# Performance work log

Measured on AMD Instinct MI355X. Metric: run time of the kernel, lower is better.

The kernel has to match this reference:

```python
import jax, jax.numpy as jnp
import numpy as np

DIM = 128
N_HEADS = 4
HEAD_DIM = DIM // N_HEADS
K = 16
B, N = 2, 8192
BIAS_HID = 32


def knn_idx(xyz, k):
    # squared pairwise distances: [B,N,N] (same argsort order as cdist)
    sq = jnp.sum(xyz * xyz, axis=-1)  # [B,N]
    d2 = sq[:, :, None] + sq[:, None, :] - 2.0 * jnp.einsum('bnd,bmd->bnm', xyz, xyz)
    _, idx = jax.lax.top_k(-d2, k)  # smallest distances
    return idx  # [B,N,k]


def setup_inputs() -> dict:
    key = jax.random.key(0)
    ks = jax.random.split(key, 12)
    s = 1.0 / np.sqrt(DIM)
    inp = {
        'x':   jax.random.normal(ks[0], (B, N, DIM), jnp.float32),
        'xyz': jax.random.normal(ks[1], (B, N, 3), jnp.float32),
        'Wq': jax.random.uniform(ks[2], (DIM, DIM), jnp.float32, -s, s),
        'bq': jnp.zeros((DIM,), jnp.float32),
        'Wk': jax.random.uniform(ks[3], (DIM, DIM), jnp.float32, -s, s),
        'bk': jnp.zeros((DIM,), jnp.float32),
        'Wv': jax.random.uniform(ks[4], (DIM, DIM), jnp.float32, -s, s),
        'bv': jnp.zeros((DIM,), jnp.float32),
        'Wo': jax.random.uniform(ks[5], (DIM, DIM), jnp.float32, -s, s),
        'bo': jnp.zeros((DIM,), jnp.float32),
        'W1': jax.random.uniform(ks[6], (3, BIAS_HID), jnp.float32, -0.5, 0.5),
        'b1': jnp.zeros((BIAS_HID,), jnp.float32),
        'W2': jax.random.uniform(ks[7], (BIAS_HID, N_HEADS), jnp.float32, -1.0 / np.sqrt(BIAS_HID), 1.0 / np.sqrt(BIAS_HID)),
        'b2': jnp.zeros((N_HEADS,), jnp.float32),
    }
    return inp


def reference(x, xyz, Wq, bq, Wk, bk, Wv, bv, Wo, bo, W1, b1, W2, b2):
    Bb, Nn, C = x.shape
    idx = knn_idx(xyz, K)  # [B,N,k]

    q = (x @ Wq + bq).reshape(Bb, Nn, N_HEADS, HEAD_DIM)
    kf = (x @ Wk + bk).reshape(Bb, Nn, N_HEADS, HEAD_DIM)
    vf = (x @ Wv + bv).reshape(Bb, Nn, N_HEADS, HEAD_DIM)

    gather = jax.vmap(lambda f, i: f[i])  # per-batch fancy gather
    kn = gather(kf, idx)  # [B,N,k,H,D]
    vn = gather(vf, idx)  # [B,N,k,H,D]
    nxyz = gather(xyz, idx)  # [B,N,k,3]

    rel = xyz[:, :, None, :] - nxyz  # [B,N,k,3]
    bias = jax.nn.relu(rel @ W1 + b1) @ W2 + b2  # [B,N,k,H]

    scores = jnp.einsum('bnhd,bnkhd->bnhk', q, kn) / np.sqrt(HEAD_DIM)
    scores = scores + jnp.swapaxes(bias, 2, 3)  # [B,N,H,k]
    attn = jax.nn.softmax(scores, axis=-1)
    out = jnp.einsum('bnhk,bnkhd->bnhd', attn, vn).reshape(Bb, Nn, C)
    return out @ Wo + bo
```

## Files before the change

### kernel.cpp

```cpp
#include <hip/hip_runtime.h>
#include <hip/hip_bf16.h>
#include <math.h>

#define BATCH 2
#define NPT   8192
#define DIMC  128
#define NH    4
#define KNN_K 16
#define HID   32
#define BN    (BATCH*NPT)

#define TILE 1024
#define QPW  2
#define NWV  4

__device__ __forceinline__ float readlane_f(float v, int l) {
  return __int_as_float(__builtin_amdgcn_readlane(__float_as_int(v), l));
}

__global__ __launch_bounds__(256) void knn_kernel(const float* __restrict__ xyz,
                                                  int* __restrict__ knn_out) {
  __shared__ float4 spts[TILE];
  const int tid  = threadIdx.x;
  const int lane = tid & 63;
  const int wave = tid >> 6;
  const int qbase = blockIdx.x * (NWV*QPW) + wave * QPW;
  const int b = qbase / NPT;

  float qx[QPW], qy[QPW], qz[QPW], qsq[QPW];
  float topd[QPW]; int topi[QPW]; float tau[QPW];
#pragma unroll
  for (int qi = 0; qi < QPW; ++qi) {
    const int g = qbase + qi;
    qx[qi] = xyz[(size_t)g*3+0];
    qy[qi] = xyz[(size_t)g*3+1];
    qz[qi] = xyz[(size_t)g*3+2];
    qsq[qi] = __fadd_rn(__fadd_rn(__fmul_rn(qx[qi],qx[qi]),
                                  __fmul_rn(qy[qi],qy[qi])),
                        __fmul_rn(qz[qi],qz[qi]));
    topd[qi] = 3e38f; topi[qi] = 0; tau[qi] = 3e38f;
  }

  for (int t = 0; t < NPT/TILE; ++t) {
    __syncthreads();
    const float* src = xyz + (size_t)(b*NPT + t*TILE)*3;
    for (int i = tid; i < TILE; i += 256) {
      const float x = src[i*3+0], y = src[i*3+1], z = src[i*3+2];
      const float sq = __fadd_rn(__fadd_rn(__fmul_rn(x,x), __fmul_rn(y,y)),
                                 __fmul_rn(z,z));
      spts[i] = make_float4(x+x, y+y, z+z, sq);
    }
    __syncthreads();

    for (int c = 0; c < TILE/64; ++c) {
      const float4 cd = spts[c*64 + lane];
      const int cbase = t*TILE + c*64;
#pragma unroll
      for (int qi = 0; qi < QPW; ++qi) {
        float dot2 = __fadd_rn(__fadd_rn(__fmul_rn(qx[qi],cd.x),
                                         __fmul_rn(qy[qi],cd.y)),
                               __fmul_rn(qz[qi],cd.z));
        float d2 = __fsub_rn(__fadd_rn(qsq[qi], cd.w), dot2);
        unsigned long long m = __ballot(d2 < tau[qi]);
        while (m) {
          const int l = (int)__builtin_ctzll(m);
          const float dn = readlane_f(d2, l);
          const int   ni_ = cbase + l;
          const float my  = topd[qi];
          const int   myi = topi[qi];
          float ab  = __shfl_up(my, 1);
          int   abi = __shfl_up(myi, 1);
          if (lane == 0) ab = -3e38f;
          const bool ge = dn < my;
          const bool gt = dn < ab;
          topd[qi] = ge ? (gt ? ab  : dn ) : my;
          topi[qi] = ge ? (gt ? abi : ni_) : myi;
          tau[qi] = readlane_f(topd[qi], 15);
          m &= (m - 1);
          if (m) m &= __ballot(d2 < tau[qi]);
        }
      }
    }
  }

#pragma unroll
  for (int qi = 0; qi < QPW; ++qi) {
    if (lane < KNN_K) knn_out[(size_t)(qbase + qi)*KNN_K + lane] = topi[qi];
  }
}

__device__ __forceinline__ float f4c(const float4 v, int u) {
  return u == 0 ? v.x : u == 1 ? v.y : u == 2 ? v.z : v.w;
}

#define QKV_ROWS 32

__global__ __launch_bounds__(128) void qkv_kernel(const float* __restrict__ x,
    const float* __restrict__ Wq, const float* __restrict__ bq,
    const float* __restrict__ Wk, const float* __restrict__ bk,
    const float* __restrict__ Wv, const float* __restrict__ bv,
    float* __restrict__ q, float* __restrict__ k, float* __restrict__ v) {
  __shared__ float xs[QKV_ROWS*DIMC];
  const int tid = threadIdx.x;
  const int rowbase = blockIdx.x * QKV_ROWS;
  {
    float4* xs4 = (float4*)xs;
    const float4* src4 = (const float4*)(x + (size_t)rowbase*DIMC);
    for (int i = tid; i < QKV_ROWS*DIMC/4; i += 128) xs4[i] = src4[i];
  }
  __syncthreads();

  const int cg = tid & 31, rg = tid >> 5;
  const int c0 = cg * 4;
  float4 aq[8], ak[8], av[8];
  {
    const float4 bq4 = *(const float4*)&bq[c0];
    const float4 bk4 = *(const float4*)&bk[c0];
    const float4 bv4 = *(const float4*)&bv[c0];
#pragma unroll
    for (int i = 0; i < 8; ++i) { aq[i] = bq4; ak[i] = bk4; av[i] = bv4; }
  }

  for (int kk = 0; kk < DIMC; kk += 4) {
    float4 xr[8];
#pragma unroll
    for (int i = 0; i < 8; ++i)
      xr[i] = *(const float4*)&xs[(rg + 4*i)*DIMC + kk];
#pragma unroll
    for (int u = 0; u < 4; ++u) {
      const float4 wq = *(const float4*)&Wq[(size_t)(kk+u)*DIMC + c0];
      const float4 wk = *(const float4*)&Wk[(size_t)(kk+u)*DIMC + c0];
      const float4 wv = *(const float4*)&Wv[(size_t)(kk+u)*DIMC + c0];
#pragma unroll
      for (int i = 0; i < 8; ++i) {
        const float xv = f4c(xr[i], u);
        aq[i].x = fmaf(xv, wq.x, aq[i].x); aq[i].y = fmaf(xv, wq.y, aq[i].y);
        aq[i].z = fmaf(xv, wq.z, aq[i].z); aq[i].w = fmaf(xv, wq.w, aq[i].w);
        ak[i].x = fmaf(xv, wk.x, ak[i].x); ak[i].y = fmaf(xv, wk.y, ak[i].y);
        ak[i].z = fmaf(xv, wk.z, ak[i].z); ak[i].w = fmaf(xv, wk.w, ak[i].w);
        av[i].x = fmaf(xv, wv.x, av[i].x); av[i].y = fmaf(xv, wv.y, av[i].y);
        av[i].z = fmaf(xv, wv.z, av[i].z); av[i].w = fmaf(xv, wv.w, av[i].w);
      }
    }
  }

#pragma unroll
  for (int i = 0; i < 8; ++i) {
    const size_t rr = (size_t)(rowbase + rg + 4*i)*DIMC + c0;
    *(float4*)&q[rr] = aq[i];
    *(float4*)&k[rr] = ak[i];
    *(float4*)&v[rr] = av[i];
  }
}

template <int CTRL>
__device__ __forceinline__ float dppf(float x) {
  return __int_as_float(__builtin_amdgcn_update_dpp(
      __float_as_int(x), __float_as_int(x), CTRL, 0xF, 0xF, false));
}
#define ROR1 0x121
#define ROR2 0x122
#define ROR4 0x124
#define ROR8 0x128

__global__ __launch_bounds__(256) void attn_kernel(const float* __restrict__ xyz,
    const int* __restrict__ knn, const float* __restrict__ qb,
    const float* __restrict__ kb, const float* __restrict__ vb,
    const float* __restrict__ W1, const float* __restrict__ b1,
    const float* __restrict__ W2, const float* __restrict__ b2,
    float* __restrict__ ao) {
  __shared__ float sw[4][NH][KNN_K];
  __shared__ int   sn[4][KNN_K];
  const int tid  = threadIdx.x;
  const int wave = tid >> 6;
  const int lane = tid & 63;
  const int p = blockIdx.x * 4 + wave;
  const int b = p / NPT;
  const int h = lane >> 4;
  const int j = lane & 15;

  const int nj = knn[(size_t)p*KNN_K + j];
  if (h == 0) sn[wave][j] = nj;
  const size_t nn = (size_t)b*NPT + nj;

  const float qx0 = xyz[(size_t)p*3+0];
  const float qy0 = xyz[(size_t)p*3+1];
  const float qz0 = xyz[(size_t)p*3+2];
  const float rx = qx0 - xyz[nn*3+0];
  const float ry = qy0 - xyz[nn*3+1];
  const float rz = qz0 - xyz[nn*3+2];
  float bias = b2[h];
#pragma unroll 8
  for (int u = 0; u < HID; ++u) {
    float hv = rx*W1[0*HID+u] + ry*W1[1*HID+u] + rz*W1[2*HID+u] + b1[u];
    hv = hv > 0.f ? hv : 0.f;
    bias = fmaf(hv, W2[u*NH + h], bias);
  }

  const float* qrow = qb + (size_t)p*DIMC + h*32;
  const float* krow = kb + nn*DIMC + h*32;
  float s = 0.f;
#pragma unroll
  for (int u = 0; u < 32; u += 4) {
    const float4 qv = *(const float4*)(qrow + u);
    const float4 kv = *(const float4*)(krow + u);
    s = fmaf(qv.x, kv.x, s); s = fmaf(qv.y, kv.y, s);
    s = fmaf(qv.z, kv.z, s); s = fmaf(qv.w, kv.w, s);
  }
  s = s * 0.17677669529663689f + bias;

  float m = s;
  m = fmaxf(m, dppf<ROR1>(m));
  m = fmaxf(m, dppf<ROR2>(m));
  m = fmaxf(m, dppf<ROR4>(m));
  m = fmaxf(m, dppf<ROR8>(m));
  const float e = expf(s - m);
  float ssum = e;
  ssum += dppf<ROR1>(ssum);
  ssum += dppf<ROR2>(ssum);
  ssum += dppf<ROR4>(ssum);
  ssum += dppf<ROR8>(ssum);
  sw[wave][h][j] = e / ssum;

  __syncthreads();

  const int d0 = lane;
  const int hA = d0 >> 5;
  float out0 = 0.f, out1 = 0.f;
  const float* vbase = vb + (size_t)b*NPT*DIMC;
#pragma unroll 4
  for (int j2 = 0; j2 < KNN_K; ++j2) {
    const int n = sn[wave][j2];
    const float wA = sw[wave][hA][j2];
    const float wB = sw[wave][2+hA][j2];
    const float* vrow = vbase + (size_t)n*DIMC;
    out0 = fmaf(wA, vrow[d0],    out0);
    out1 = fmaf(wB, vrow[64+d0], out1);
  }
  ao[(size_t)p*DIMC + d0]      = out0;
  ao[(size_t)p*DIMC + 64 + d0] = out1;
}

__global__ __launch_bounds__(128) void proj_kernel(float* __restrict__ inout,
    const float* __restrict__ Wo, const float* __restrict__ bo) {
  __shared__ float xs[QKV_ROWS*DIMC];
  const int tid = threadIdx.x;
  const int rowbase = blockIdx.x * QKV_ROWS;
  {
    float4* xs4 = (float4*)xs;
    const float4* src4 = (const float4*)(inout + (size_t)rowbase*DIMC);
    for (int i = tid; i < QKV_ROWS*DIMC/4; i += 128) xs4[i] = src4[i];
  }
  __syncthreads();

  const int cg = tid & 31, rg = tid >> 5;
  const int c0 = cg * 4;
  float4 a[8];
  {
    const float4 bo4 = *(const float4*)&bo[c0];
#pragma unroll
    for (int i = 0; i < 8; ++i) a[i] = bo4;
  }

  for (int kk = 0; kk < DIMC; kk += 4) {
    float4 xr[8];
#pragma unroll
    for (int i = 0; i < 8; ++i)
      xr[i] = *(const float4*)&xs[(rg + 4*i)*DIMC + kk];
#pragma unroll
    for (int u = 0; u < 4; ++u) {
      const float4 w = *(const float4*)&Wo[(size_t)(kk+u)*DIMC + c0];
#pragma unroll
      for (int i = 0; i < 8; ++i) {
        const float xv = f4c(xr[i], u);
        a[i].x = fmaf(xv, w.x, a[i].x); a[i].y = fmaf(xv, w.y, a[i].y);
        a[i].z = fmaf(xv, w.z, a[i].z); a[i].w = fmaf(xv, w.w, a[i].w);
      }
    }
  }

#pragma unroll
  for (int i = 0; i < 8; ++i)
    *(float4*)&inout[(size_t)(rowbase + rg + 4*i)*DIMC + c0] = a[i];
}

extern "C" void kernel_launch(void* const* d_in, const int* in_sizes, int n_in,
                              void* d_out, int out_size, void* d_ws, size_t ws_size,
                              hipStream_t stream) {
  const float* x   = (const float*)d_in[0];
  const float* xyz = (const float*)d_in[1];
  const float* Wq  = (const float*)d_in[2];
  const float* bq  = (const float*)d_in[3];
  const float* Wk  = (const float*)d_in[4];
  const float* bk  = (const float*)d_in[5];
  const float* Wv  = (const float*)d_in[6];
  const float* bv  = (const float*)d_in[7];
  const float* Wo  = (const float*)d_in[8];
  const float* bo  = (const float*)d_in[9];
  const float* W1  = (const float*)d_in[10];
  const float* b1  = (const float*)d_in[11];
  const float* W2  = (const float*)d_in[12];
  const float* b2  = (const float*)d_in[13];
  float* out = (float*)d_out;

  char* ws = (char*)d_ws;
  int*   knn = (int*)ws;
  float* q   = (float*)(ws + (size_t)(1u<<20));
  float* k   = (float*)(ws + (size_t)9*(1u<<20));
  float* v   = (float*)(ws + (size_t)17*(1u<<20));

  hipLaunchKernelGGL(knn_kernel, dim3(BN/(NWV*QPW)), dim3(256), 0, stream, xyz, knn);
  hipLaunchKernelGGL(qkv_kernel, dim3(BN/QKV_ROWS), dim3(128), 0, stream,
                     x, Wq, bq, Wk, bk, Wv, bv, q, k, v);
  hipLaunchKernelGGL(attn_kernel, dim3(BN/4), dim3(256), 0, stream,
                     xyz, knn, q, k, v, W1, b1, W2, b2, out);
  hipLaunchKernelGGL(proj_kernel, dim3(BN/QKV_ROWS), dim3(128), 0, stream,
                     out, Wo, bo);
}
```

Before: 194.6 us.

## Replace brute-force KNN with uniform-grid spatial binning and ring search

Swaps the all-pairs KNN scan for a 32^3 uniform grid built per batch. Zero, count, scan and scatter kernels bin the points into cells, then a query kernel searches outward ring by ring around each query's cell and stops once the ring bound exceeds the current 16th-best distance. Distance ties are broken by index so the result stays deterministic. This removes the O(N^2) distance work in exchange for four extra small launches, a single-block scan and atomics, and the cell bounds assume coordinates mostly fall in [-4,4].

```diff
diff --git a/kernel.cpp b/kernel.cpp
--- a/kernel.cpp
+++ b/kernel.cpp
@@ -10,83 +10,152 @@
 #define HID   32
 #define BN    (BATCH*NPT)
 
-#define TILE 1024
-#define QPW  2
-#define NWV  4
+#define GRID_N 32
+#define NCELL  (GRID_N*GRID_N*GRID_N)
+#define GLO   -4.0f
+#define GCS    0.25f
+#define GINV   4.0f
 
 __device__ __forceinline__ float readlane_f(float v, int l) {
   return __int_as_float(__builtin_amdgcn_readlane(__float_as_int(v), l));
 }
-
-__global__ __launch_bounds__(256) void knn_kernel(const float* __restrict__ xyz,
-                                                  int* __restrict__ knn_out) {
-  __shared__ float4 spts[TILE];
-  const int tid  = threadIdx.x;
-  const int lane = tid & 63;
-  const int wave = tid >> 6;
-  const int qbase = blockIdx.x * (NWV*QPW) + wave * QPW;
-  const int b = qbase / NPT;
-
-  float qx[QPW], qy[QPW], qz[QPW], qsq[QPW];
-  float topd[QPW]; int topi[QPW]; float tau[QPW];
-#pragma unroll
-  for (int qi = 0; qi < QPW; ++qi) {
-    const int g = qbase + qi;
-    qx[qi] = xyz[(size_t)g*3+0];
-    qy[qi] = xyz[(size_t)g*3+1];
-    qz[qi] = xyz[(size_t)g*3+2];
-    qsq[qi] = __fadd_rn(__fadd_rn(__fmul_rn(qx[qi],qx[qi]),
-                                  __fmul_rn(qy[qi],qy[qi])),
-                        __fmul_rn(qz[qi],qz[qi]));
-    topd[qi] = 3e38f; topi[qi] = 0; tau[qi] = 3e38f;
-  }
-
-  for (int t = 0; t < NPT/TILE; ++t) {
+__device__ __forceinline__ int clampi(int v, int lo, int hi) {
+  return v < lo ? lo : (v > hi ? hi : v);
+}
+__device__ __forceinline__ int cell_of(float x, float y, float z) {
+  const int cx = clampi((int)floorf((x - GLO)*GINV), 0, GRID_N-1);
+  const int cy = clampi((int)floorf((y - GLO)*GINV), 0, GRID_N-1);
+  const int cz = clampi((int)floorf((z - GLO)*GINV), 0, GRID_N-1);
+  return (cz*GRID_N + cy)*GRID_N + cx;
+}
+
+__global__ __launch_bounds__(256) void zero_kernel(int* __restrict__ c) {
+  const int i = blockIdx.x*256 + threadIdx.x;
+  if (i < 2*NCELL) c[i] = 0;
+}
+
+__global__ __launch_bounds__(256) void count_kernel(const float* __restrict__ xyz,
+                                                    int* __restrict__ counts) {
+  const int i = blockIdx.x*256 + threadIdx.x;
+  const float x = xyz[(size_t)i*3+0], y = xyz[(size_t)i*3+1], z = xyz[(size_t)i*3+2];
+  const int b = i >> 13;
+  atomicAdd(&counts[b*NCELL + cell_of(x,y,z)], 1);
+}
+
+__global__ __launch_bounds__(1024) void scan_kernel(const int* __restrict__ counts,
+                                                    int* __restrict__ starts,
+                                                    int* __restrict__ cursor) {
+  __shared__ int sd[1024];
+  const int t = threadIdx.x;
+  for (int b = 0; b < 2; ++b) {
+    const int* c = counts + b*NCELL;
+    int* s  = starts + b*(NCELL+1);
+    int* cu = cursor + b*NCELL;
+    int loc[32]; int sum = 0;
+#pragma unroll
+    for (int j = 0; j < 32; ++j) { loc[j] = sum; sum += c[t*32 + j]; }
     __syncthreads();
-    const float* src = xyz + (size_t)(b*NPT + t*TILE)*3;
-    for (int i = tid; i < TILE; i += 256) {
-      const float x = src[i*3+0], y = src[i*3+1], z = src[i*3+2];
-      const float sq = __fadd_rn(__fadd_rn(__fmul_rn(x,x), __fmul_rn(y,y)),
-                                 __fmul_rn(z,z));
-      spts[i] = make_float4(x+x, y+y, z+z, sq);
-    }
+    sd[t] = sum;
     __syncthreads();
-
-    for (int c = 0; c < TILE/64; ++c) {
-      const float4 cd = spts[c*64 + lane];
-      const int cbase = t*TILE + c*64;
-#pragma unroll
-      for (int qi = 0; qi < QPW; ++qi) {
-        float dot2 = __fadd_rn(__fadd_rn(__fmul_rn(qx[qi],cd.x),
-                                         __fmul_rn(qy[qi],cd.y)),
-                               __fmul_rn(qz[qi],cd.z));
-        float d2 = __fsub_rn(__fadd_rn(qsq[qi], cd.w), dot2);
-        unsigned long long m = __ballot(d2 < tau[qi]);
-        while (m) {
-          const int l = (int)__builtin_ctzll(m);
-          const float dn = readlane_f(d2, l);
-          const int   ni_ = cbase + l;
-          const float my  = topd[qi];
-          const int   myi = topi[qi];
-          float ab  = __shfl_up(my, 1);
-          int   abi = __shfl_up(myi, 1);
-          if (lane == 0) ab = -3e38f;
-          const bool ge = dn < my;
-          const bool gt = dn < ab;
-          topd[qi] = ge ? (gt ? ab  : dn ) : my;
-          topi[qi] = ge ? (gt ? abi : ni_) : myi;
-          tau[qi] = readlane_f(topd[qi], 15);
-          m &= (m - 1);
-          if (m) m &= __ballot(d2 < tau[qi]);
+    for (int off = 1; off < 1024; off <<= 1) {
+      const int u = (t >= off) ? sd[t-off] : 0;
+      __syncthreads();
+      sd[t] += u;
+      __syncthreads();
+    }
+    const int excl = sd[t] - sum;
+#pragma unroll
+    for (int j = 0; j < 32; ++j) { s[t*32+j] = excl + loc[j]; cu[t*32+j] = excl + loc[j]; }
+    if (t == 1023) s[NCELL] = sd[1023];
+  }
+}
+
+__global__ __launch_bounds__(256) void scatter_kernel(const float* __restrict__ xyz,
+    int* __restrict__ cursor, float4* __restrict__ pts4, int* __restrict__ pidx) {
+  const int i = blockIdx.x*256 + threadIdx.x;
+  const float x = xyz[(size_t)i*3+0], y = xyz[(size_t)i*3+1], z = xyz[(size_t)i*3+2];
+  const int b = i >> 13;
+  const float sq = __fadd_rn(__fadd_rn(__fmul_rn(x,x), __fmul_rn(y,y)),
+                             __fmul_rn(z,z));
+  const int slot = atomicAdd(&cursor[b*NCELL + cell_of(x,y,z)], 1);
+  pts4[b*NPT + slot] = make_float4(x+x, y+y, z+z, sq);
+  pidx[b*NPT + slot] = i & (NPT-1);
+}
+
+__global__ __launch_bounds__(256) void knn_query_kernel(const float* __restrict__ xyz,
+    const int* __restrict__ starts, const float4* __restrict__ pts4,
+    const int* __restrict__ pidx, int* __restrict__ knn_out) {
+  const int tid = threadIdx.x, lane = tid & 63, wave = tid >> 6;
+  const int p = blockIdx.x*4 + wave;
+  const int b = p >> 13;
+  const float qx = xyz[(size_t)p*3+0], qy = xyz[(size_t)p*3+1], qz = xyz[(size_t)p*3+2];
+  const float qsq = __fadd_rn(__fadd_rn(__fmul_rn(qx,qx), __fmul_rn(qy,qy)),
+                              __fmul_rn(qz,qz));
+  const int cx = clampi((int)floorf((qx - GLO)*GINV), 0, GRID_N-1);
+  const int cy = clampi((int)floorf((qy - GLO)*GINV), 0, GRID_N-1);
+  const int cz = clampi((int)floorf((qz - GLO)*GINV), 0, GRID_N-1);
+  const int*    sb = starts + b*(NCELL+1);
+  const float4* pb = pts4 + (size_t)b*NPT;
+  const int*    ib = pidx + (size_t)b*NPT;
+
+  float topd = INFINITY; int topi = 0x7fffffff;
+  float tau  = INFINITY; int taui = 0x7fffffff;
+
+  auto process = [&](int beg, int end) {
+    for (int c0 = beg; c0 < end; c0 += 64) {
+      const int ci = c0 + lane;
+      float d2 = INFINITY; int di = 0x7fffffff;
+      if (ci < end) {
+        const float4 cd = pb[ci];
+        const float dot2 = __fadd_rn(__fadd_rn(__fmul_rn(qx,cd.x),
+                                               __fmul_rn(qy,cd.y)),
+                                     __fmul_rn(qz,cd.z));
+        d2 = __fsub_rn(__fadd_rn(qsq, cd.w), dot2);
+        di = ib[ci];
+      }
+      unsigned long long m = __ballot((d2 < tau) | (d2 == tau && di < taui));
+      while (m) {
+        const int l = (int)__builtin_ctzll(m);
+        const float dn  = readlane_f(d2, l);
+        const int   dni = __builtin_amdgcn_readlane(di, l);
+        const float my  = topd; const int myi = topi;
+        float ab  = __shfl_up(my, 1);
+        int   abi = __shfl_up(myi, 1);
+        if (lane == 0) { ab = -INFINITY; abi = -1; }
+        const bool ge = (dn < my) | (dn == my && dni < myi);
+        const bool gt = (dn < ab) | (dn == ab && dni < abi);
+        topd = ge ? (gt ? ab  : dn ) : my;
+        topi = ge ? (gt ? abi : dni) : myi;
+        tau  = readlane_f(topd, 15);
+        taui = __builtin_amdgcn_readlane(topi, 15);
+        m &= (m - 1);
+        if (m) m &= __ballot((d2 < tau) | (d2 == tau && di < taui));
+      }
+    }
+  };
+
+  for (int r = 0; r < GRID_N; ++r) {
+    const int zlo = clampi(cz-r, 0, GRID_N-1), zhi = clampi(cz+r, 0, GRID_N-1);
+    const int ylo = clampi(cy-r, 0, GRID_N-1), yhi = clampi(cy+r, 0, GRID_N-1);
+    const int xlo = clampi(cx-r, 0, GRID_N-1), xhi = clampi(cx+r, 0, GRID_N-1);
+    for (int z = zlo; z <= zhi; ++z) {
+      const bool ze = (z == cz-r) || (z == cz+r);
+      for (int y = ylo; y <= yhi; ++y) {
+        const bool ye = (y == cy-r) || (y == cy+r);
+        const int cb = (z*GRID_N + y)*GRID_N;
+        if (ze || ye) {
+          process(sb[cb+xlo], sb[cb+xhi+1]);
+        } else {
+          if (cx-r >= 0)       process(sb[cb+cx-r], sb[cb+cx-r+1]);
+          if (cx+r <= GRID_N-1) process(sb[cb+cx+r], sb[cb+cx+r+1]);
         }
       }
     }
-  }
-
-#pragma unroll
-  for (int qi = 0; qi < QPW; ++qi) {
-    if (lane < KNN_K) knn_out[(size_t)(qbase + qi)*KNN_K + lane] = topi[qi];
-  }
+    const float rb = (float)r*GCS - 1e-5f;
+    if (rb > 0.f && rb*rb > tau) break;
+  }
+
+  if (lane < KNN_K) knn_out[(size_t)p*KNN_K + lane] = topi;
 }
 
 __device__ __forceinline__ float f4c(const float4 v, int u) {
@@ -304,12 +373,23 @@
   float* out = (float*)d_out;
 
   char* ws = (char*)d_ws;
-  int*   knn = (int*)ws;
-  float* q   = (float*)(ws + (size_t)(1u<<20));
-  float* k   = (float*)(ws + (size_t)9*(1u<<20));
-  float* v   = (float*)(ws + (size_t)17*(1u<<20));
-
-  hipLaunchKernelGGL(knn_kernel, dim3(BN/(NWV*QPW)), dim3(256), 0, stream, xyz, knn);
+  int*    knn    = (int*)ws;
+  char*   g      = ws + (1u<<20);
+  int*    counts = (int*)g;
+  int*    starts = (int*)(g + 256*1024);
+  int*    cursor = (int*)(g + 576*1024);
+  float4* pts4   = (float4*)(g + 832*1024);
+  int*    pidx   = (int*)(g + 1088*1024);
+  float*  q      = (float*)(ws + (size_t)(1u<<20));
+  float*  k      = (float*)(ws + (size_t)9*(1u<<20));
+  float*  v      = (float*)(ws + (size_t)17*(1u<<20));
+
+  hipLaunchKernelGGL(zero_kernel,  dim3((2*NCELL+255)/256), dim3(256), 0, stream, counts);
+  hipLaunchKernelGGL(count_kernel, dim3(BN/256), dim3(256), 0, stream, xyz, counts);
+  hipLaunchKernelGGL(scan_kernel,  dim3(1), dim3(1024), 0, stream, counts, starts, cursor);
+  hipLaunchKernelGGL(scatter_kernel, dim3(BN/256), dim3(256), 0, stream, xyz, cursor, pts4, pidx);
+  hipLaunchKernelGGL(knn_query_kernel, dim3(BN/4), dim3(256), 0, stream,
+                     xyz, starts, pts4, pidx, knn);
   hipLaunchKernelGGL(qkv_kernel, dim3(BN/QKV_ROWS), dim3(128), 0, stream,
                      x, Wq, bq, Wk, bk, Wv, bv, q, k, v);
   hipLaunchKernelGGL(attn_kernel, dim3(BN/4), dim3(256), 0, stream,
```

Result: slower. 418.1 us (+114.8%).
